# Performance work log

Measured on AMD Instinct MI355X. Metric: run time of the kernel, lower is better.

Reference implementation:

```python
import jax, jax.numpy as jnp
import numpy as np

N, E, U, DEPTH = 50000, 800000, 64, 4
NODE_F, EDGE_F = 2, 1
EPS = 1e-5


def setup_inputs() -> dict:
    key = jax.random.key(0)
    ks = jax.random.split(key, 20)
    s = lambda k, shape, fan_in: jax.random.normal(k, shape, jnp.float32) * (1.0 / np.sqrt(fan_in))
    inp = {
        "x": jax.random.normal(ks[0], (N, NODE_F), jnp.float32),
        "edge_index": jax.random.randint(ks[1], (2, E), 0, N, jnp.int32),
        "edge_attr": jax.random.uniform(ks[2], (E, EDGE_F), jnp.float32),
        # input projections
        "node_W": s(ks[3], (NODE_F, U), NODE_F),
        "node_b": jnp.zeros((U,), jnp.float32),
        "edge_W": s(ks[4], (EDGE_F, U), EDGE_F),
        "edge_b": jnp.zeros((U,), jnp.float32),
        # per-layer message MLP: Linear(2U->U), SiLU, Linear(U->U)
        "msg_W1": s(ks[5], (DEPTH, 2 * U, U), 2 * U),
        "msg_b1": jnp.zeros((DEPTH, U), jnp.float32),
        "msg_W2": s(ks[6], (DEPTH, U, U), U),
        "msg_b2": jnp.zeros((DEPTH, U), jnp.float32),
        # per-layer update MLP: Linear(2U->U), SiLU, Linear(U->U)
        "upd_W1": s(ks[7], (DEPTH, 2 * U, U), 2 * U),
        "upd_b1": jnp.zeros((DEPTH, U), jnp.float32),
        "upd_W2": s(ks[8], (DEPTH, U, U), U),
        "upd_b2": jnp.zeros((DEPTH, U), jnp.float32),
        # per-layer LayerNorm
        "ln_g": jnp.ones((DEPTH, U), jnp.float32),
        "ln_b": jnp.zeros((DEPTH, U), jnp.float32),
    }
    return inp


def reference(x, edge_index, edge_attr, node_W, node_b, edge_W, edge_b,
              msg_W1, msg_b1, msg_W2, msg_b2,
              upd_W1, upd_b1, upd_W2, upd_b2, ln_g, ln_b):
    silu = jax.nn.silu
    n = x.shape[0]
    src = edge_index[0]  # x_j (source, gathered)
    dst = edge_index[1]  # aggregation target i

    h = silu(x @ node_W + node_b)           # (n, U)
    e = silu(edge_attr @ edge_W + edge_b)   # (E, U)

    # mean aggregation denominator (in-degree, clamped to 1 as PyG does)
    deg = jax.ops.segment_sum(jnp.ones((src.shape[0],), h.dtype), dst, num_segments=n)
    deg = jnp.maximum(deg, 1.0)[:, None]

    for i in range(DEPTH):
        # message: msg_mlp(cat[x_j, edge_attr])
        m = jnp.concatenate([h[src], e], axis=-1)               # (E, 2U)
        m = silu(m @ msg_W1[i] + msg_b1[i]) @ msg_W2[i] + msg_b2[i]  # (E, U)
        # aggregate: mean over incoming edges
        aggr = jax.ops.segment_sum(m, dst, num_segments=n) / deg     # (n, U)
        # update: update_mlp(cat[x, aggr_out])
        u = jnp.concatenate([h, aggr], axis=-1)                 # (n, 2U)
        h_new = silu(u @ upd_W1[i] + upd_b1[i]) @ upd_W2[i] + upd_b2[i]
        # residual + LayerNorm
        h = h + h_new
        mu = jnp.mean(h, axis=-1, keepdims=True)
        var = jnp.mean(jnp.square(h - mu), axis=-1, keepdims=True)
        h = (h - mu) * jax.lax.rsqrt(var + EPS) * ln_g[i] + ln_b[i]
    return h
```

## Files before the change

### kernel.cpp

```cpp
#include <hip/hip_runtime.h>
#include <hip/hip_fp16.h>

#define NN 50000
#define NE 800000
#define DEPTH 4
#define EPSF 1e-5f
#define GTAB 8192
#define GROWS (GTAB + 1)
#define NWAVE 8192
#define NBKT 196
#define BK_BLOCKS 256
#define EPB (NE / BK_BLOCKS)
#define CSR_MAXE 8192

typedef _Float16 f16;
typedef _Float16 f16x8 __attribute__((ext_vector_type(8)));
typedef float f32x4 __attribute__((ext_vector_type(4)));

#define MFMA16(a, b, c) __builtin_amdgcn_mfma_f32_16x16x32_f16(a, b, c, 0, 0, 0)

static __device__ __forceinline__ float silu_f(float x) {
    float e = __builtin_amdgcn_exp2f(x * -1.44269504088896f);
    return x * __builtin_amdgcn_rcpf(1.0f + e);
}

#define WT_TOTAL (2 * DEPTH * (8192 + 4096))

__global__ void k_prep0(const float* __restrict__ mW1, const float* __restrict__ mW2,
                        const float* __restrict__ uW1, const float* __restrict__ uW2,
                        f16* __restrict__ w1t, f16* __restrict__ w2t,
                        f16* __restrict__ u1t, f16* __restrict__ u2t,
                        const float* __restrict__ x, const float* __restrict__ nW,
                        const float* __restrict__ nb,
                        float* __restrict__ h32, f16* __restrict__ h16) {
    int i = blockIdx.x * 256 + threadIdx.x;
    const int A = DEPTH * 8192, B = DEPTH * 4096;
    if (i < WT_TOTAL) {
        const float* src; f16* dst; int K, rel;
        if (i < A)              { src = mW1; dst = w1t; K = 128; rel = i; }
        else if (i < A + B)     { src = mW2; dst = w2t; K = 64;  rel = i - A; }
        else if (i < 2 * A + B) { src = uW1; dst = u1t; K = 128; rel = i - A - B; }
        else                    { src = uW2; dst = u2t; K = 64;  rel = i - 2 * A - B; }
        int kc = K * 64;
        int d = rel / kc, r = rel - d * kc;
        int k = r / 64, c = r - k * 64;
        dst[d * kc + c * K + k] = (f16)src[rel];
    } else {
        int j = i - WT_TOTAL;
        if (j >= NN * 64) return;
        int n = j >> 6, u = j & 63;
        float v = silu_f(fmaf(x[2 * n], nW[u], fmaf(x[2 * n + 1], nW[64 + u], nb[u])));
        h32[j] = v;
        h16[j] = (f16)v;
    }
}

__global__ __launch_bounds__(256)
void k_bhist(const int* __restrict__ ei, int* __restrict__ ghist) {
    __shared__ int hist[NBKT];
    int tid = threadIdx.x;
    for (int i = tid; i < NBKT; i += 256) hist[i] = 0;
    __syncthreads();
    int base = blockIdx.x * EPB;
    for (int it = 0; it < EPB; it += 256) {
        if (it + tid < EPB) atomicAdd(&hist[ei[NE + base + it + tid] >> 8], 1);
    }
    __syncthreads();
    for (int b = tid; b < NBKT; b += 256)
        ghist[b * BK_BLOCKS + blockIdx.x] = hist[b];
}

__global__ __launch_bounds__(256)
void k_bscan1(int* __restrict__ ghist, int* __restrict__ tot) {
    int tid = threadIdx.x, lane = tid & 63, w = tid >> 6;
    int b = blockIdx.x * 4 + w;
    if (b >= NBKT) return;
    int carry = 0;
    #pragma unroll
    for (int c = 0; c < 4; ++c) {
        int idx = b * BK_BLOCKS + c * 64 + lane;
        int v = ghist[idx];
        int incl = v;
        #pragma unroll
        for (int off = 1; off < 64; off <<= 1) {
            int t = __shfl_up(incl, off, 64);
            if (lane >= off) incl += t;
        }
        ghist[idx] = incl - v + carry;
        carry += __shfl(incl, 63, 64);
    }
    if (lane == 0) tot[b] = carry;
}

__global__ void k_bscan2(const int* __restrict__ tot, int* __restrict__ bstart) {
    __shared__ int t[NBKT];
    int tid = threadIdx.x;
    if (tid < NBKT) t[tid] = tot[tid];
    __syncthreads();
    if (tid <= NBKT) {
        int s = 0;
        for (int j = 0; j < tid && j < NBKT; ++j) s += t[j];
        bstart[tid] = s;
    }
}

__global__ __launch_bounds__(256)
void k_bscatter(const int* __restrict__ ei, const float* __restrict__ ea,
                const int* __restrict__ goff, const int* __restrict__ bstart,
                unsigned long long* __restrict__ btmp) {
    __shared__ int hist[NBKT], lbase[NBKT], cur[NBKT], gbase[NBKT];
    __shared__ unsigned long long stg[EPB];
    int tid = threadIdx.x;
    for (int i = tid; i < NBKT; i += 256) hist[i] = 0;
    __syncthreads();
    int base = blockIdx.x * EPB;
    for (int it = 0; it < EPB; it += 256) {
        if (it + tid < EPB) atomicAdd(&hist[ei[NE + base + it + tid] >> 8], 1);
    }
    __syncthreads();
    if (tid == 0) {
        int run = 0;
        for (int b = 0; b < NBKT; ++b) { lbase[b] = run; cur[b] = run; run += hist[b]; }
    }
    __syncthreads();
    if (tid < NBKT) gbase[tid] = goff[tid * BK_BLOCKS + blockIdx.x] + bstart[tid];
    __syncthreads();
    for (int it = 0; it < EPB; it += 256) {
        if (it + tid < EPB) {
            int j = base + it + tid;
            int d = ei[NE + j];
            int src = ei[j];
            int gi = (int)fmaf(ea[j], (float)GTAB, 0.5f);
            gi = gi > GTAB ? GTAB : gi;
            unsigned long long e = ((unsigned long long)(unsigned int)d << 32)
                                 | ((unsigned long long)(((unsigned int)gi << 16) | (unsigned int)src));
            int p = atomicAdd(&cur[d >> 8], 1);
            stg[p] = e;
        }
    }
    __syncthreads();
    for (int i = tid; i < EPB; i += 256) {
        unsigned long long e = stg[i];
        int b = (int)(e >> 40);
        btmp[gbase[b] + (i - lbase[b])] = e;
    }
}

__global__ __launch_bounds__(1024)
void k_csr(const unsigned long long* __restrict__ btmp, const int* __restrict__ bstart,
           int* __restrict__ rowptr, unsigned int* __restrict__ epack) {
    __shared__ int hist[256], sbase[256], cur[256];
    __shared__ unsigned int stg[CSR_MAXE];
    int tid = threadIdx.x;
    int b = blockIdx.x;
    int e0 = bstart[b], e1 = bstart[b + 1];
    int ne = e1 - e0;
    int n0 = b << 8;
    int nn = NN - n0; if (nn > 256) nn = 256;
    if (tid < 256) hist[tid] = 0;
    __syncthreads();
    for (int i = tid; i < ne; i += 1024)
        atomicAdd(&hist[(int)(btmp[e0 + i] >> 32) - n0], 1);
    __syncthreads();
    if (tid == 0) {
        int run = e0;
        for (int i = 0; i < 256; ++i) { sbase[i] = run; cur[i] = run - e0; run += hist[i]; }
    }
    __syncthreads();
    if (tid < nn) rowptr[n0 + tid] = sbase[tid];
    if (b == NBKT - 1 && tid == 0) rowptr[NN] = NE;
    bool fits = (ne <= CSR_MAXE);
    for (int i = tid; i < ne; i += 1024) {
        unsigned long long e = btmp[e0 + i];
        int local = (int)(e >> 32) - n0;
        int p = atomicAdd(&cur[local], 1);
        if (fits) stg[p] = (unsigned int)e;
        else epack[e0 + p] = (unsigned int)e;
    }
    __syncthreads();
    if (fits)
        for (int i = tid; i < ne; i += 1024) epack[e0 + i] = stg[i];
}

__global__ void k_wstart(const int* __restrict__ rowptr, int* __restrict__ wstart) {
    int w = blockIdx.x * 256 + threadIdx.x;
    if (w > NWAVE) return;
    int target = (int)(((long long)w * NE) / NWAVE);
    int lo = 0, hi = NN;
    while (lo < hi) {
        int mid = (lo + hi) >> 1;
        if (rowptr[mid] >= target) hi = mid; else lo = mid + 1;
    }
    wstart[w] = lo;
}

__global__ void k_gtab(const float* __restrict__ eW, const float* __restrict__ eb,
                       const float* __restrict__ mb1, const float* __restrict__ mW1,
                       f16* __restrict__ G) {
    __shared__ float es[4][64];
    int tid = threadIdx.x;
    int w = tid >> 6, lane = tid & 63;
    int rowid = blockIdx.x * 4 + w;
    if (rowid >= DEPTH * GROWS) return;
    int l = rowid / GROWS, i = rowid - l * GROWS;
    float x = (float)i * (1.0f / GTAB);
    es[w][lane] = silu_f(fmaf(x, eW[lane], eb[lane]));
    float s = mb1[l * 64 + lane];
    const float* Wl = mW1 + (size_t)l * 8192;
    #pragma unroll 8
    for (int u = 0; u < 64; ++u)
        s = fmaf(es[w][u], Wl[(64 + u) * 64 + lane], s);
    G[(size_t)rowid * 64 + lane] = (f16)s;
}

#define HP_TILES 3125
#define HP_BLOCKS 391

__global__ __launch_bounds__(512, 4)
void k_hprime(const f16* __restrict__ h16, const f16* __restrict__ w1t,
              f16* __restrict__ hp16) {
    __shared__ f16 wa[64 * 64];
    int tid = threadIdx.x;
    {
        int g = tid;
        int c = g >> 3, k0 = (g & 7) << 3;
        f16x8 v = *(const f16x8*)&w1t[c * 128 + k0];
        *(f16x8*)&wa[(c << 6) | (k0 ^ ((c & 7) << 3))] = v;
    }
    __syncthreads();

    int w = tid >> 6, lane = tid & 63;
    int row = lane & 15, g4 = lane >> 4;

    int tile = blockIdx.x * 8 + w;
    if (tile >= HP_TILES) return;
    int n0 = tile * 16;
    int nA = n0 + row;

    f16x8 ha0 = *(const f16x8*)&h16[(size_t)nA * 64 + g4 * 8];
    f16x8 ha1 = *(const f16x8*)&h16[(size_t)nA * 64 + 32 + g4 * 8];

    int nC = n0 + g4 * 4;
    #pragma unroll
    for (int cb = 0; cb < 4; ++cb) {
        int c = row + 16 * cb;
        f32x4 acc = (f32x4){0.f, 0.f, 0.f, 0.f};
        f16x8 wb0 = *(const f16x8*)&wa[(c << 6) | ((g4 * 8) ^ ((c & 7) << 3))];
        f16x8 wb1 = *(const f16x8*)&wa[(c << 6) | ((32 + g4 * 8) ^ ((c & 7) << 3))];
        acc = MFMA16(ha0, wb0, acc);
        acc = MFMA16(ha1, wb1, acc);
        #pragma unroll
        for (int v = 0; v < 4; ++v)
            hp16[(size_t)(nC + v) * 64 + c] = (f16)acc[v];
    }
}

#define EK_BLOCKS (NWAVE / 4)

__global__ __launch_bounds__(256, 8)
void k_edge(const int* __restrict__ rowptr, const int* __restrict__ wstart,
            const unsigned int* __restrict__ epack,
            const f16* __restrict__ hp16, const f16* __restrict__ G0,
            f16* __restrict__ Sm) {
    int tid = threadIdx.x;
    int w = tid >> 6, lane = tid & 63;

    int gw = blockIdx.x * 4 + w;
    int nbeg = wstart[gw], nend = wstart[gw + 1];

    for (int n = nbeg; n < nend; ++n) {
        int kb0 = rowptr[n], ke = rowptr[n + 1];
        if (ke <= kb0) continue;
        float acc = 0.f;
        int p = kb0;

        for (; p + 8 <= ke; p += 8) {
            unsigned int k0 = epack[p],     k1 = epack[p + 1],
                         k2 = epack[p + 2], k3 = epack[p + 3],
                         k4 = epack[p + 4], k5 = epack[p + 5],
                         k6 = epack[p + 6], k7 = epack[p + 7];
            float hv0 = (float)hp16[(size_t)(k0 & 0xFFFFu) * 64 + lane];
            float hv1 = (float)hp16[(size_t)(k1 & 0xFFFFu) * 64 + lane];
            float hv2 = (float)hp16[(size_t)(k2 & 0xFFFFu) * 64 + lane];
            float hv3 = (float)hp16[(size_t)(k3 & 0xFFFFu) * 64 + lane];
            float hv4 = (float)hp16[(size_t)(k4 & 0xFFFFu) * 64 + lane];
            float hv5 = (float)hp16[(size_t)(k5 & 0xFFFFu) * 64 + lane];
            float hv6 = (float)hp16[(size_t)(k6 & 0xFFFFu) * 64 + lane];
            float hv7 = (float)hp16[(size_t)(k7 & 0xFFFFu) * 64 + lane];
            float g0 = (float)G0[(size_t)(k0 >> 16) * 64 + lane];
            float g1 = (float)G0[(size_t)(k1 >> 16) * 64 + lane];
            float g2 = (float)G0[(size_t)(k2 >> 16) * 64 + lane];
            float g3 = (float)G0[(size_t)(k3 >> 16) * 64 + lane];
            float g4v = (float)G0[(size_t)(k4 >> 16) * 64 + lane];
            float g5 = (float)G0[(size_t)(k5 >> 16) * 64 + lane];
            float g6 = (float)G0[(size_t)(k6 >> 16) * 64 + lane];
            float g7 = (float)G0[(size_t)(k7 >> 16) * 64 + lane];
            acc += silu_f(hv0 + g0) + silu_f(hv1 + g1)
                 + silu_f(hv2 + g2) + silu_f(hv3 + g3)
                 + silu_f(hv4 + g4v) + silu_f(hv5 + g5)
                 + silu_f(hv6 + g6) + silu_f(hv7 + g7);
        }
        for (; p + 4 <= ke; p += 4) {
            unsigned int k0 = epack[p],     k1 = epack[p + 1],
                         k2 = epack[p + 2], k3 = epack[p + 3];
            float hv0 = (float)hp16[(size_t)(k0 & 0xFFFFu) * 64 + lane];
            float hv1 = (float)hp16[(size_t)(k1 & 0xFFFFu) * 64 + lane];
            float hv2 = (float)hp16[(size_t)(k2 & 0xFFFFu) * 64 + lane];
            float hv3 = (float)hp16[(size_t)(k3 & 0xFFFFu) * 64 + lane];
            float g0 = (float)G0[(size_t)(k0 >> 16) * 64 + lane];
            float g1 = (float)G0[(size_t)(k1 >> 16) * 64 + lane];
            float g2 = (float)G0[(size_t)(k2 >> 16) * 64 + lane];
            float g3 = (float)G0[(size_t)(k3 >> 16) * 64 + lane];
            acc += silu_f(hv0 + g0) + silu_f(hv1 + g1)
                 + silu_f(hv2 + g2) + silu_f(hv3 + g3);
        }
        for (; p < ke; ++p) {
            unsigned int k0 = epack[p];
            acc += silu_f((float)hp16[(size_t)(k0 & 0xFFFFu) * 64 + lane]
                        + (float)G0[(size_t)(k0 >> 16) * 64 + lane]);
        }
        float m = acc * __builtin_amdgcn_rcpf((float)(ke - kb0));
        Sm[(size_t)n * 64 + lane] = (f16)m;
    }
}

#define NK_TILES 3125
#define NK_BLOCKS 391

__global__ __launch_bounds__(512, 6)
void k_node(const f16* __restrict__ h16, const float* __restrict__ h32,
            const f16* __restrict__ Sm, const int* __restrict__ rowptr,
            const f16* __restrict__ w2t, const float* __restrict__ b2,
            const f16* __restrict__ u1t, const float* __restrict__ b1u,
            const f16* __restrict__ u2t, const float* __restrict__ b2u,
            const float* __restrict__ lng, const float* __restrict__ lnb,
            const f16* __restrict__ w1an,
            float* __restrict__ h32o, f16* __restrict__ h16o,
            f16* __restrict__ hp16o) {
    __shared__ f16 u1s[64 * 128];
    __shared__ f16 w2s[64 * 64], u2s[64 * 64];
    __shared__ float b2s[64], b1us[64], b2us[64], lngs[64], lnbs[64];
    __shared__ f16 trs[8][16 * 64];

    int tid = threadIdx.x;
    {
        const f16x8* u1v = (const f16x8*)u1t;
        #pragma unroll
        for (int it = 0; it < 2; ++it) {
            int g = tid + it * 512;
            int c = g >> 4, k0 = (g & 15) << 3;
            *(f16x8*)&u1s[(c << 7) | (k0 ^ ((c & 7) << 3))] = u1v[g];
        }
        const f16x8* w2v = (const f16x8*)w2t;
        const f16x8* u2v = (const f16x8*)u2t;
        {
            int g = tid;
            int c = g >> 3, k0 = (g & 7) << 3;
            int pp = (c << 6) | (k0 ^ ((c & 7) << 3));
            *(f16x8*)&w2s[pp] = w2v[g];
            *(f16x8*)&u2s[pp] = u2v[g];
        }
    }
    if (tid < 64) {
        b2s[tid] = b2[tid]; b1us[tid] = b1u[tid]; b2us[tid] = b2u[tid];
        lngs[tid] = lng[tid]; lnbs[tid] = lnb[tid];
    }
    __syncthreads();

    int w = tid >> 6, lane = tid & 63;
    int row = lane & 15, g4 = lane >> 4;
    f16* tp = trs[w];

    int tile = blockIdx.x * 8 + w;
    if (tile >= NK_TILES) return;
    int n0 = tile * 16;
    int nA = n0 + row;

    int degA = rowptr[nA + 1] - rowptr[nA];
    f16x8 sa0 = *(const f16x8*)&Sm[(size_t)nA * 64 + g4 * 8];
    f16x8 sa1 = *(const f16x8*)&Sm[(size_t)nA * 64 + 32 + g4 * 8];
    if (degA <= 0) {
        #pragma unroll
        for (int j = 0; j < 8; ++j) { sa0[j] = (f16)0.f; sa1[j] = (f16)0.f; }
    }
    int nC = n0 + g4 * 4;
    int r0 = rowptr[nC], r1 = rowptr[nC + 1], r2 = rowptr[nC + 2],
        r3 = rowptr[nC + 3], r4 = rowptr[nC + 4];
    float f0 = r1 > r0 ? 1.f : 0.f;
    float f1 = r2 > r1 ? 1.f : 0.f;
    float f2 = r3 > r2 ? 1.f : 0.f;
    float f3 = r4 > r3 ? 1.f : 0.f;

    f32x4 agg[4];
    #pragma unroll
    for (int cb = 0; cb < 4; ++cb) {
        int c = row + 16 * cb;
        float bv = b2s[c];
        agg[cb] = (f32x4){bv * f0, bv * f1, bv * f2, bv * f3};
        f16x8 wb0 = *(const f16x8*)&w2s[(c << 6) | ((g4 * 8) ^ ((c & 7) << 3))];
        f16x8 wb1 = *(const f16x8*)&w2s[(c << 6) | ((32 + g4 * 8) ^ ((c & 7) << 3))];
        agg[cb] = MFMA16(sa0, wb0, agg[cb]);
        agg[cb] = MFMA16(sa1, wb1, agg[cb]);
    }

    #pragma unroll
    for (int cb = 0; cb < 4; ++cb) {
        int c = row + 16 * cb;
        #pragma unroll
        for (int v = 0; v < 4; ++v) {
            int r = g4 * 4 + v;
            tp[(r << 6) | (c ^ ((r & 7) << 3))] = (f16)agg[cb][v];
        }
    }
    f16x8 ha0 = *(const f16x8*)&h16[(size_t)nA * 64 + g4 * 8];
    f16x8 ha1 = *(const f16x8*)&h16[(size_t)nA * 64 + 32 + g4 * 8];
    f16x8 aa2 = *(const f16x8*)&tp[(row << 6) | ((g4 * 8) ^ ((row & 7) << 3))];
    f16x8 aa3 = *(const f16x8*)&tp[(row << 6) | ((32 + g4 * 8) ^ ((row & 7) << 3))];

    f32x4 hid[4];
    #pragma unroll
    for (int cb = 0; cb < 4; ++cb) {
        int c = row + 16 * cb;
        float bv = b1us[c];
        hid[cb] = (f32x4){bv, bv, bv, bv};
        hid[cb] = MFMA16(ha0, *(const f16x8*)&u1s[(c << 7) | ((g4 * 8) ^ ((c & 7) << 3))], hid[cb]);
        hid[cb] = MFMA16(ha1, *(const f16x8*)&u1s[(c << 7) | ((32 + g4 * 8) ^ ((c & 7) << 3))], hid[cb]);
        hid[cb] = MFMA16(aa2, *(const f16x8*)&u1s[(c << 7) | ((64 + g4 * 8) ^ ((c & 7) << 3))], hid[cb]);
        hid[cb] = MFMA16(aa3, *(const f16x8*)&u1s[(c << 7) | ((96 + g4 * 8) ^ ((c & 7) << 3))], hid[cb]);
    }

    #pragma unroll
    for (int cb = 0; cb < 4; ++cb) {
        int c = row + 16 * cb;
        #pragma unroll
        for (int v = 0; v < 4; ++v) {
            int r = g4 * 4 + v;
            tp[(r << 6) | (c ^ ((r & 7) << 3))] = (f16)silu_f(hid[cb][v]);
        }
    }
    f16x8 za0 = *(const f16x8*)&tp[(row << 6) | ((g4 * 8) ^ ((row & 7) << 3))];
    f16x8 za1 = *(const f16x8*)&tp[(row << 6) | ((32 + g4 * 8) ^ ((row & 7) << 3))];

    f32x4 out[4];
    #pragma unroll
    for (int cb = 0; cb < 4; ++cb) {
        int c = row + 16 * cb;
        float bv = b2us[c];
        out[cb] = (f32x4){bv, bv, bv, bv};
        out[cb] = MFMA16(za0, *(const f16x8*)&u2s[(c << 6) | ((g4 * 8) ^ ((c & 7) << 3))], out[cb]);
        out[cb] = MFMA16(za1, *(const f16x8*)&u2s[(c << 6) | ((32 + g4 * 8) ^ ((c & 7) << 3))], out[cb]);
    }

    #pragma unroll
    for (int v = 0; v < 4; ++v) {
        int n = nC + v;
        float hp[4];
        float s = 0.f, q = 0.f;
        #pragma unroll
        for (int cb = 0; cb < 4; ++cb) {
            float xv = h32[(size_t)n * 64 + row + 16 * cb] + out[cb][v];
            hp[cb] = xv; s += xv; q += xv * xv;
        }
        #pragma unroll
        for (int off = 1; off < 16; off <<= 1) {
            s += __shfl_xor(s, off, 64);
            q += __shfl_xor(q, off, 64);
        }
        float mu = s * 0.015625f;
        float var = q * 0.015625f - mu * mu;
        float rstd = __builtin_amdgcn_rsqf(var + EPSF);
        int r = g4 * 4 + v;
        #pragma unroll
        for (int cb = 0; cb < 4; ++cb) {
            int c = row + 16 * cb;
            float o = (hp[cb] - mu) * rstd * lngs[c] + lnbs[c];
            h32o[(size_t)n * 64 + c] = o;
            f16 o16 = (f16)o;
            h16o[(size_t)n * 64 + c] = o16;
            tp[(r << 6) | (c ^ ((r & 7) << 3))] = o16;
        }
    }

    if (w1an) {
        f16x8 pa0 = *(const f16x8*)&tp[(row << 6) | ((g4 * 8) ^ ((row & 7) << 3))];
        f16x8 pa1 = *(const f16x8*)&tp[(row << 6) | ((32 + g4 * 8) ^ ((row & 7) << 3))];
        #pragma unroll
        for (int cb = 0; cb < 4; ++cb) {
            int c = row + 16 * cb;
            f32x4 acc = (f32x4){0.f, 0.f, 0.f, 0.f};
            f16x8 wb0 = *(const f16x8*)&w1an[c * 128 + g4 * 8];
            f16x8 wb1 = *(const f16x8*)&w1an[c * 128 + 32 + g4 * 8];
            acc = MFMA16(pa0, wb0, acc);
            acc = MFMA16(pa1, wb1, acc);
            #pragma unroll
            for (int v = 0; v < 4; ++v)
                hp16o[(size_t)(nC + v) * 64 + c] = (f16)acc[v];
        }
    }
}

extern "C" void kernel_launch(void* const* d_in, const int* in_sizes, int n_in,
                              void* d_out, int out_size, void* d_ws, size_t ws_size,
                              hipStream_t stream) {
    const float* x   = (const float*)d_in[0];
    const int*   ei  = (const int*)d_in[1];
    const float* ea  = (const float*)d_in[2];
    const float* nW  = (const float*)d_in[3];
    const float* nb  = (const float*)d_in[4];
    const float* eW  = (const float*)d_in[5];
    const float* eb  = (const float*)d_in[6];
    const float* mW1 = (const float*)d_in[7];
    const float* mb1 = (const float*)d_in[8];
    const float* mW2 = (const float*)d_in[9];
    const float* mb2 = (const float*)d_in[10];
    const float* uW1 = (const float*)d_in[11];
    const float* ub1 = (const float*)d_in[12];
    const float* uW2 = (const float*)d_in[13];
    const float* ub2 = (const float*)d_in[14];
    const float* lng = (const float*)d_in[15];
    const float* lnb = (const float*)d_in[16];

    char* p = (char*)d_ws;
    f16*   Sm     = (f16*)p;    p += (size_t)NN * 64 * 2;
    float* h32    = (float*)p;  p += (size_t)NN * 64 * 4;
    f16*   h16    = (f16*)p;    p += (size_t)NN * 64 * 2;
    f16*   hp16   = (f16*)p;    p += (size_t)NN * 64 * 2;
    int*   rowptr = (int*)p;    p += (size_t)(NN + 4) * 4;
    int*   ghist  = (int*)p;    p += (size_t)NBKT * BK_BLOCKS * 4;
    int*   tot    = (int*)p;    p += (size_t)(NBKT + 4) * 4;
    int*   bstart = (int*)p;    p += (size_t)(NBKT + 4) * 4;
    int*   wstart = (int*)p;    p += (size_t)(NWAVE + 4) * 4;
    unsigned int* epack = (unsigned int*)p; p += (size_t)NE * 4;
    unsigned long long* btmp = (unsigned long long*)p; p += (size_t)NE * 8;
    f16*   G      = (f16*)p;    p += (size_t)DEPTH * GROWS * 64 * 2;
    f16*   w1t = (f16*)p;    p += (size_t)DEPTH * 8192 * 2;
    f16*   w2t = (f16*)p;    p += (size_t)DEPTH * 4096 * 2;
    f16*   u1t = (f16*)p;    p += (size_t)DEPTH * 8192 * 2;
    f16*   u2t = (f16*)p;    p += (size_t)DEPTH * 4096 * 2;

    k_prep0<<<(WT_TOTAL + NN * 64 + 255) / 256, 256, 0, stream>>>(
        mW1, mW2, uW1, uW2, w1t, w2t, u1t, u2t, x, nW, nb, h32, h16);

    k_bhist<<<BK_BLOCKS, 256, 0, stream>>>(ei, ghist);
    k_bscan1<<<(NBKT + 3) / 4, 256, 0, stream>>>(ghist, tot);
    k_bscan2<<<1, 256, 0, stream>>>(tot, bstart);
    k_bscatter<<<BK_BLOCKS, 256, 0, stream>>>(ei, ea, ghist, bstart, btmp);
    k_csr<<<NBKT, 1024, 0, stream>>>(btmp, bstart, rowptr, epack);
    k_wstart<<<(NWAVE + 256) / 256, 256, 0, stream>>>(rowptr, wstart);
    k_gtab<<<(DEPTH * GROWS + 3) / 4, 256, 0, stream>>>(eW, eb, mb1, mW1, G);
    k_hprime<<<HP_BLOCKS, 512, 0, stream>>>(h16, w1t, hp16);

    for (int l = 0; l < DEPTH; ++l) {
        k_edge<<<EK_BLOCKS, 256, 0, stream>>>(rowptr, wstart, epack, hp16,
            G + (size_t)l * GROWS * 64, Sm);
        k_node<<<NK_BLOCKS, 512, 0, stream>>>(h16, h32, Sm, rowptr,
            w2t + (size_t)l * 4096, mb2 + l * 64,
            u1t + (size_t)l * 8192, ub1 + l * 64,
            u2t + (size_t)l * 4096, ub2 + l * 64,
            lng + l * 64, lnb + l * 64,
            (l + 1 < DEPTH) ? (w1t + (size_t)(l + 1) * 8192) : (const f16*)nullptr,
            (l == DEPTH - 1) ? (float*)d_out : h32, h16, hp16);
    }
}
```

Before: 271.7 us.

## Merge prep kernels, fold wstart search into edge kernel, drop fp32 residual

Folds the weight conversion, G table build and bucket histogram into one launch, and fuses the two scan kernels into a single-block scan. The per-wave binary search for node ranges now runs inside the edge kernel instead of a separate wstart kernel. The fp32 copy of h is removed, so the residual is read from the fp16 copy and only the last layer writes fp32 output. This cuts launch count and memory traffic, but adds a redundant binary search per edge-kernel launch and lowers residual precision to fp16.

```diff
diff --git a/kernel.cpp b/kernel.cpp
--- a/kernel.cpp
+++ b/kernel.cpp
@@ -25,82 +25,112 @@
 }
 
 #define WT_TOTAL (2 * DEPTH * (8192 + 4096))
-
-__global__ void k_prep0(const float* __restrict__ mW1, const float* __restrict__ mW2,
-                        const float* __restrict__ uW1, const float* __restrict__ uW2,
-                        f16* __restrict__ w1t, f16* __restrict__ w2t,
-                        f16* __restrict__ u1t, f16* __restrict__ u2t,
-                        const float* __restrict__ x, const float* __restrict__ nW,
-                        const float* __restrict__ nb,
-                        float* __restrict__ h32, f16* __restrict__ h16) {
-    int i = blockIdx.x * 256 + threadIdx.x;
-    const int A = DEPTH * 8192, B = DEPTH * 4096;
-    if (i < WT_TOTAL) {
-        const float* src; f16* dst; int K, rel;
-        if (i < A)              { src = mW1; dst = w1t; K = 128; rel = i; }
-        else if (i < A + B)     { src = mW2; dst = w2t; K = 64;  rel = i - A; }
-        else if (i < 2 * A + B) { src = uW1; dst = u1t; K = 128; rel = i - A - B; }
-        else                    { src = uW2; dst = u2t; K = 64;  rel = i - 2 * A - B; }
-        int kc = K * 64;
-        int d = rel / kc, r = rel - d * kc;
-        int k = r / 64, c = r - k * 64;
-        dst[d * kc + c * K + k] = (f16)src[rel];
+#define NB_P0 ((WT_TOTAL + NN * 64 + 255) / 256)
+#define NB_GT ((DEPTH * GROWS + 3) / 4)
+#define NB_BH BK_BLOCKS
+#define NB_PREP (NB_P0 + NB_GT + NB_BH)
+
+__global__ void k_prep(const float* __restrict__ mW1, const float* __restrict__ mW2,
+                       const float* __restrict__ uW1, const float* __restrict__ uW2,
+                       f16* __restrict__ w1t, f16* __restrict__ w2t,
+                       f16* __restrict__ u1t, f16* __restrict__ u2t,
+                       const float* __restrict__ x, const float* __restrict__ nW,
+                       const float* __restrict__ nb, f16* __restrict__ h16,
+                       const float* __restrict__ eW, const float* __restrict__ eb,
+                       const float* __restrict__ mb1, f16* __restrict__ G,
+                       const int* __restrict__ ei, int* __restrict__ ghist) {
+    __shared__ int hist[NBKT];
+    __shared__ float es[4][64];
+    int blk = blockIdx.x;
+    int tid = threadIdx.x;
+
+    if (blk < NB_P0) {
+        int i = blk * 256 + tid;
+        const int A = DEPTH * 8192, B = DEPTH * 4096;
+        if (i < WT_TOTAL) {
+            const float* src; f16* dst; int K, rel;
+            if (i < A)              { src = mW1; dst = w1t; K = 128; rel = i; }
+            else if (i < A + B)     { src = mW2; dst = w2t; K = 64;  rel = i - A; }
+            else if (i < 2 * A + B) { src = uW1; dst = u1t; K = 128; rel = i - A - B; }
+            else                    { src = uW2; dst = u2t; K = 64;  rel = i - 2 * A - B; }
+            int kc = K * 64;
+            int d = rel / kc, r = rel - d * kc;
+            int k = r / 64, c = r - k * 64;
+            dst[d * kc + c * K + k] = (f16)src[rel];
+        } else {
+            int j = i - WT_TOTAL;
+            if (j < NN * 64) {
+                int n = j >> 6, u = j & 63;
+                h16[j] = (f16)silu_f(fmaf(x[2 * n], nW[u],
+                                          fmaf(x[2 * n + 1], nW[64 + u], nb[u])));
+            }
+        }
+    } else if (blk < NB_P0 + NB_GT) {
+        int w = tid >> 6, lane = tid & 63;
+        int rowid = (blk - NB_P0) * 4 + w;
+        if (rowid < DEPTH * GROWS) {
+            int l = rowid / GROWS, i = rowid - l * GROWS;
+            float xv = (float)i * (1.0f / GTAB);
+            es[w][lane] = silu_f(fmaf(xv, eW[lane], eb[lane]));
+            float s = mb1[l * 64 + lane];
+            const float* Wl = mW1 + (size_t)l * 8192;
+            #pragma unroll 8
+            for (int u = 0; u < 64; ++u)
+                s = fmaf(es[w][u], Wl[(64 + u) * 64 + lane], s);
+            G[(size_t)rowid * 64 + lane] = (f16)s;
+        }
     } else {
-        int j = i - WT_TOTAL;
-        if (j >= NN * 64) return;
-        int n = j >> 6, u = j & 63;
-        float v = silu_f(fmaf(x[2 * n], nW[u], fmaf(x[2 * n + 1], nW[64 + u], nb[u])));
-        h32[j] = v;
-        h16[j] = (f16)v;
-    }
-}
-
-__global__ __launch_bounds__(256)
-void k_bhist(const int* __restrict__ ei, int* __restrict__ ghist) {
-    __shared__ int hist[NBKT];
-    int tid = threadIdx.x;
-    for (int i = tid; i < NBKT; i += 256) hist[i] = 0;
-    __syncthreads();
-    int base = blockIdx.x * EPB;
-    for (int it = 0; it < EPB; it += 256) {
-        if (it + tid < EPB) atomicAdd(&hist[ei[NE + base + it + tid] >> 8], 1);
-    }
-    __syncthreads();
-    for (int b = tid; b < NBKT; b += 256)
-        ghist[b * BK_BLOCKS + blockIdx.x] = hist[b];
-}
-
-__global__ __launch_bounds__(256)
-void k_bscan1(int* __restrict__ ghist, int* __restrict__ tot) {
+        int b = blk - NB_P0 - NB_GT;
+        for (int i = tid; i < NBKT; i += 256) hist[i] = 0;
+        __syncthreads();
+        int base = b * EPB;
+        for (int it = 0; it < EPB; it += 256) {
+            if (it + tid < EPB) atomicAdd(&hist[ei[NE + base + it + tid] >> 8], 1);
+        }
+        __syncthreads();
+        for (int bb = tid; bb < NBKT; bb += 256)
+            ghist[bb * BK_BLOCKS + b] = hist[bb];
+    }
+}
+
+__global__ __launch_bounds__(1024)
+void k_bscan(int* __restrict__ ghist, int* __restrict__ bstart) {
+    __shared__ int tot[NBKT];
     int tid = threadIdx.x, lane = tid & 63, w = tid >> 6;
-    int b = blockIdx.x * 4 + w;
-    if (b >= NBKT) return;
-    int carry = 0;
-    #pragma unroll
-    for (int c = 0; c < 4; ++c) {
-        int idx = b * BK_BLOCKS + c * 64 + lane;
-        int v = ghist[idx];
-        int incl = v;
-        #pragma unroll
-        for (int off = 1; off < 64; off <<= 1) {
-            int t = __shfl_up(incl, off, 64);
-            if (lane >= off) incl += t;
-        }
-        ghist[idx] = incl - v + carry;
-        carry += __shfl(incl, 63, 64);
-    }
-    if (lane == 0) tot[b] = carry;
-}
-
-__global__ void k_bscan2(const int* __restrict__ tot, int* __restrict__ bstart) {
-    __shared__ int t[NBKT];
-    int tid = threadIdx.x;
-    if (tid < NBKT) t[tid] = tot[tid];
-    __syncthreads();
-    if (tid <= NBKT) {
-        int s = 0;
-        for (int j = 0; j < tid && j < NBKT; ++j) s += t[j];
-        bstart[tid] = s;
+    for (int b = w; b < NBKT; b += 16) {
+        int carry = 0;
+        #pragma unroll
+        for (int c = 0; c < 4; ++c) {
+            int idx = b * BK_BLOCKS + c * 64 + lane;
+            int v = ghist[idx];
+            int incl = v;
+            #pragma unroll
+            for (int off = 1; off < 64; off <<= 1) {
+                int t = __shfl_up(incl, off, 64);
+                if (lane >= off) incl += t;
+            }
+            ghist[idx] = incl - v + carry;
+            carry += __shfl(incl, 63, 64);
+        }
+        if (lane == 0) tot[b] = carry;
+    }
+    __syncthreads();
+    if (tid < 64) {
+        int carry = 0;
+        #pragma unroll
+        for (int c = 0; c < 4; ++c) {
+            int i = c * 64 + tid;
+            int v = (i < NBKT) ? tot[i] : 0;
+            int incl = v;
+            #pragma unroll
+            for (int off = 1; off < 64; off <<= 1) {
+                int t = __shfl_up(incl, off, 64);
+                if (tid >= off) incl += t;
+            }
+            if (i < NBKT) bstart[i] = incl - v + carry;
+            carry += __shfl(incl, 63, 64);
+        }
+        if (tid == 0) bstart[NBKT] = carry;
     }
 }
 
@@ -182,37 +212,6 @@
         for (int i = tid; i < ne; i += 1024) epack[e0 + i] = stg[i];
 }
 
-__global__ void k_wstart(const int* __restrict__ rowptr, int* __restrict__ wstart) {
-    int w = blockIdx.x * 256 + threadIdx.x;
-    if (w > NWAVE) return;
-    int target = (int)(((long long)w * NE) / NWAVE);
-    int lo = 0, hi = NN;
-    while (lo < hi) {
-        int mid = (lo + hi) >> 1;
-        if (rowptr[mid] >= target) hi = mid; else lo = mid + 1;
-    }
-    wstart[w] = lo;
-}
-
-__global__ void k_gtab(const float* __restrict__ eW, const float* __restrict__ eb,
-                       const float* __restrict__ mb1, const float* __restrict__ mW1,
-                       f16* __restrict__ G) {
-    __shared__ float es[4][64];
-    int tid = threadIdx.x;
-    int w = tid >> 6, lane = tid & 63;
-    int rowid = blockIdx.x * 4 + w;
-    if (rowid >= DEPTH * GROWS) return;
-    int l = rowid / GROWS, i = rowid - l * GROWS;
-    float x = (float)i * (1.0f / GTAB);
-    es[w][lane] = silu_f(fmaf(x, eW[lane], eb[lane]));
-    float s = mb1[l * 64 + lane];
-    const float* Wl = mW1 + (size_t)l * 8192;
-    #pragma unroll 8
-    for (int u = 0; u < 64; ++u)
-        s = fmaf(es[w][u], Wl[(64 + u) * 64 + lane], s);
-    G[(size_t)rowid * 64 + lane] = (f16)s;
-}
-
 #define HP_TILES 3125
 #define HP_BLOCKS 391
 
@@ -258,15 +257,21 @@
 #define EK_BLOCKS (NWAVE / 4)
 
 __global__ __launch_bounds__(256, 8)
-void k_edge(const int* __restrict__ rowptr, const int* __restrict__ wstart,
-            const unsigned int* __restrict__ epack,
+void k_edge(const int* __restrict__ rowptr, const unsigned int* __restrict__ epack,
             const f16* __restrict__ hp16, const f16* __restrict__ G0,
             f16* __restrict__ Sm) {
     int tid = threadIdx.x;
     int w = tid >> 6, lane = tid & 63;
-
     int gw = blockIdx.x * 4 + w;
-    int nbeg = wstart[gw], nend = wstart[gw + 1];
+
+    int target = (int)(((long long)(gw + (lane & 1)) * NE) / NWAVE);
+    int lo = 0, hi = NN;
+    while (lo < hi) {
+        int mid = (lo + hi) >> 1;
+        if (rowptr[mid] >= target) hi = mid; else lo = mid + 1;
+    }
+    int nbeg = __shfl(lo, 0, 64);
+    int nend = __shfl(lo, 1, 64);
 
     for (int n = nbeg; n < nend; ++n) {
         int kb0 = rowptr[n], ke = rowptr[n + 1];
@@ -328,15 +333,15 @@
 #define NK_BLOCKS 391
 
 __global__ __launch_bounds__(512, 6)
-void k_node(const f16* __restrict__ h16, const float* __restrict__ h32,
-            const f16* __restrict__ Sm, const int* __restrict__ rowptr,
+void k_node(const f16* __restrict__ h16, const f16* __restrict__ Sm,
+            const int* __restrict__ rowptr,
             const f16* __restrict__ w2t, const float* __restrict__ b2,
             const f16* __restrict__ u1t, const float* __restrict__ b1u,
             const f16* __restrict__ u2t, const float* __restrict__ b2u,
             const float* __restrict__ lng, const float* __restrict__ lnb,
             const f16* __restrict__ w1an,
-            float* __restrict__ h32o, f16* __restrict__ h16o,
-            f16* __restrict__ hp16o) {
+            f16* __restrict__ h16o, f16* __restrict__ hp16o,
+            float* __restrict__ out32) {
     __shared__ f16 u1s[64 * 128];
     __shared__ f16 w2s[64 * 64], u2s[64 * 64];
     __shared__ float b2s[64], b1us[64], b2us[64], lngs[64], lnbs[64];
@@ -458,7 +463,7 @@
         float s = 0.f, q = 0.f;
         #pragma unroll
         for (int cb = 0; cb < 4; ++cb) {
-            float xv = h32[(size_t)n * 64 + row + 16 * cb] + out[cb][v];
+            float xv = (float)h16[(size_t)n * 64 + row + 16 * cb] + out[cb][v];
             hp[cb] = xv; s += xv; q += xv * xv;
         }
         #pragma unroll
@@ -474,9 +479,9 @@
         for (int cb = 0; cb < 4; ++cb) {
             int c = row + 16 * cb;
             float o = (hp[cb] - mu) * rstd * lngs[c] + lnbs[c];
-            h32o[(size_t)n * 64 + c] = o;
+            if (out32) out32[(size_t)n * 64 + c] = o;
             f16 o16 = (f16)o;
-            h16o[(size_t)n * 64 + c] = o16;
+            if (h16o) h16o[(size_t)n * 64 + c] = o16;
             tp[(r << 6) | (c ^ ((r & 7) << 3))] = o16;
         }
     }
@@ -522,14 +527,11 @@
 
     char* p = (char*)d_ws;
     f16*   Sm     = (f16*)p;    p += (size_t)NN * 64 * 2;
-    float* h32    = (float*)p;  p += (size_t)NN * 64 * 4;
     f16*   h16    = (f16*)p;    p += (size_t)NN * 64 * 2;
     f16*   hp16   = (f16*)p;    p += (size_t)NN * 64 * 2;
     int*   rowptr = (int*)p;    p += (size_t)(NN + 4) * 4;
     int*   ghist  = (int*)p;    p += (size_t)NBKT * BK_BLOCKS * 4;
-    int*   tot    = (int*)p;    p += (size_t)(NBKT + 4) * 4;
     int*   bstart = (int*)p;    p += (size_t)(NBKT + 4) * 4;
-    int*   wstart = (int*)p;    p += (size_t)(NWAVE + 4) * 4;
     unsigned int* epack = (unsigned int*)p; p += (size_t)NE * 4;
     unsigned long long* btmp = (unsigned long long*)p; p += (size_t)NE * 8;
     f16*   G      = (f16*)p;    p += (size_t)DEPTH * GROWS * 64 * 2;
@@ -538,27 +540,24 @@
     f16*   u1t = (f16*)p;    p += (size_t)DEPTH * 8192 * 2;
     f16*   u2t = (f16*)p;    p += (size_t)DEPTH * 4096 * 2;
 
-    k_prep0<<<(WT_TOTAL + NN * 64 + 255) / 256, 256, 0, stream>>>(
-        mW1, mW2, uW1, uW2, w1t, w2t, u1t, u2t, x, nW, nb, h32, h16);
-
-    k_bhist<<<BK_BLOCKS, 256, 0, stream>>>(ei, ghist);
-    k_bscan1<<<(NBKT + 3) / 4, 256, 0, stream>>>(ghist, tot);
-    k_bscan2<<<1, 256, 0, stream>>>(tot, bstart);
+    k_prep<<<NB_PREP, 256, 0, stream>>>(mW1, mW2, uW1, uW2, w1t, w2t, u1t, u2t,
+                                        x, nW, nb, h16, eW, eb, mb1, G, ei, ghist);
+    k_bscan<<<1, 1024, 0, stream>>>(ghist, bstart);
     k_bscatter<<<BK_BLOCKS, 256, 0, stream>>>(ei, ea, ghist, bstart, btmp);
     k_csr<<<NBKT, 1024, 0, stream>>>(btmp, bstart, rowptr, epack);
-    k_wstart<<<(NWAVE + 256) / 256, 256, 0, stream>>>(rowptr, wstart);
-    k_gtab<<<(DEPTH * GROWS + 3) / 4, 256, 0, stream>>>(eW, eb, mb1, mW1, G);
     k_hprime<<<HP_BLOCKS, 512, 0, stream>>>(h16, w1t, hp16);
 
     for (int l = 0; l < DEPTH; ++l) {
-        k_edge<<<EK_BLOCKS, 256, 0, stream>>>(rowptr, wstart, epack, hp16,
+        bool last = (l == DEPTH - 1);
+        k_edge<<<EK_BLOCKS, 256, 0, stream>>>(rowptr, epack, hp16,
             G + (size_t)l * GROWS * 64, Sm);
-        k_node<<<NK_BLOCKS, 512, 0, stream>>>(h16, h32, Sm, rowptr,
+        k_node<<<NK_BLOCKS, 512, 0, stream>>>(h16, Sm, rowptr,
             w2t + (size_t)l * 4096, mb2 + l * 64,
             u1t + (size_t)l * 8192, ub1 + l * 64,
             u2t + (size_t)l * 4096, ub2 + l * 64,
             lng + l * 64, lnb + l * 64,
-            (l + 1 < DEPTH) ? (w1t + (size_t)(l + 1) * 8192) : (const f16*)nullptr,
-            (l == DEPTH - 1) ? (float*)d_out : h32, h16, hp16);
-    }
-}
+            last ? (const f16*)nullptr : (w1t + (size_t)(l + 1) * 8192),
+            last ? (f16*)nullptr : h16, hp16,
+            last ? (float*)d_out : (float*)nullptr);
+    }
+}
```

Result: slower. 289.8 us (+6.6%).
